# Kernel tuning notes

Measured on AMD Instinct MI355X. Metric: run time of the kernel, lower is better.

The kernel has to match this reference:

```python
import jax, jax.numpy as jnp
import numpy as np

B, N, D = 2, 4096, 1024
HID, OUT = 1024, 1
APPERTURE = 256
EPS = 1e-6
Q_SCALE = 0.06


def _ln(x, g, b):
    # torch.std defaults to unbiased (ddof=1); eps added to std, not var
    mean = x.mean(-1, keepdims=True)
    std = jnp.std(x, axis=-1, ddof=1, keepdims=True)
    return g * (x - mean) / (std + EPS) + b


def _self_attn(x, Wk, Wq, Wv, Wo):
    K = x @ Wk.T
    Q = (x @ Wq.T) * Q_SCALE
    V = x @ Wv.T
    logits = jnp.einsum('bnd,bmd->bnm', Q, K)  # [B,N,N]
    idx = jnp.arange(N)
    keep = jnp.abs(idx[:, None] - idx[None, :]) < APPERTURE  # band kept
    logits = jnp.where(keep[None], logits, -jnp.inf)
    w = jax.nn.softmax(logits, axis=-1)
    # torch: y = (V^T @ w)^T  == w^T applied column-wise -> einsum over first attn index
    y = jnp.einsum('bmn,bmd->bnd', w, V)
    return y @ Wo.T


def setup_inputs() -> dict:
    key = jax.random.key(0)
    ks = jax.random.split(key, 20)
    s = 0.02
    inp = {
        'x1': jax.random.normal(ks[0], (B, N, D), jnp.float32),
        'x2': jax.random.normal(ks[1], (B, N, D), jnp.float32),
        'x3': jax.random.normal(ks[2], (B, N, D), jnp.float32),
        'Wk': jax.random.normal(ks[3], (D, D), jnp.float32) * s,
        'Wq': jax.random.normal(ks[4], (D, D), jnp.float32) * s,
        'Wv': jax.random.normal(ks[5], (D, D), jnp.float32) * s,
        'Wo': jax.random.normal(ks[6], (D, D), jnp.float32) * s,
        'ka_w': jax.random.normal(ks[7], (HID, D), jnp.float32) * s,
        'ka_b': jnp.zeros((HID,), jnp.float32),
        'kb_w': jax.random.normal(ks[8], (HID, HID), jnp.float32) * s,
        'kb_b': jnp.zeros((HID,), jnp.float32),
        'kc_w': jax.random.normal(ks[9], (HID, HID), jnp.float32) * s,
        'kc_b': jnp.zeros((HID,), jnp.float32),
        'kd_w': jax.random.normal(ks[10], (OUT, HID), jnp.float32) * s,
        'kd_b': jnp.zeros((OUT,), jnp.float32),
        'g1': jnp.ones((D,), jnp.float32),
        'b1': jnp.zeros((D,), jnp.float32),
        'g2': jnp.ones((HID,), jnp.float32),
        'b2': jnp.zeros((HID,), jnp.float32),
    }
    return inp


def reference(x1, x2, x3, Wk, Wq, Wv, Wo, ka_w, ka_b, kb_w, kb_b,
              kc_w, kc_b, kd_w, kd_b, g1, b1, g2, b2):
    # dropout in eval mode -> identity
    y = jnp.zeros_like(x1)
    for x in (x1, x2, x3):
        a = _self_attn(x, Wk, Wq, Wv, Wo)
        y = y + _ln(a + x, g1, b1)
    y = y @ ka_w.T + ka_b
    y = y @ kb_w.T + kb_b
    y = y @ kc_w.T + kc_b
    y = jax.nn.relu(y)
    y = _ln(y, g2, b2)
    y = y @ kd_w.T + kd_b  # [B,N,1]
    return y.reshape(y.shape[0], -1)  # [B,N]
```

## Files before the change

### kernel.cpp

```cpp
#include <hip/hip_runtime.h>

#define NSEQ 4096
#define DDIM 1024
#define NROWS 8192
#define NROWS3 24576
#define BAND 512
#define BM 128
#define BN 128
#define BKT 64
#define PT_W 768
#define PT_CH 64

typedef __attribute__((ext_vector_type(8))) __bf16 bf16x8;
typedef __attribute__((ext_vector_type(4))) float f32x4;

__device__ __forceinline__ unsigned short f2b(float f) {
  unsigned int u = __float_as_uint(f);
  unsigned int r = (u + 0x7FFFu + ((u >> 16) & 1u)) >> 16;
  return (unsigned short)r;
}
__device__ __forceinline__ float b2f(unsigned short b) {
  return __uint_as_float(((unsigned int)b) << 16);
}

__device__ __forceinline__ void gload16(const unsigned short* g, unsigned short* l) {
  __builtin_amdgcn_global_load_lds(
      (const __attribute__((address_space(1))) void*)g,
      (__attribute__((address_space(3))) void*)l, 16, 0, 0);
}

__device__ __forceinline__ float blk_sum(float v) {
  __shared__ float red_s[4];
  #pragma unroll
  for (int o = 32; o; o >>= 1) v += __shfl_xor(v, o);
  __syncthreads();
  if ((threadIdx.x & 63) == 0) red_s[threadIdx.x >> 6] = v;
  __syncthreads();
  return red_s[0] + red_s[1] + red_s[2] + red_s[3];
}
__device__ __forceinline__ float blk_max(float v) {
  __shared__ float red_m[4];
  #pragma unroll
  for (int o = 32; o; o >>= 1) v = fmaxf(v, __shfl_xor(v, o));
  __syncthreads();
  if ((threadIdx.x & 63) == 0) red_m[threadIdx.x >> 6] = v;
  __syncthreads();
  return fmaxf(fmaxf(red_m[0], red_m[1]), fmaxf(red_m[2], red_m[3]));
}

__global__ __launch_bounds__(256) void k_cvt(const float* __restrict__ src,
                                             unsigned short* __restrict__ dst,
                                             int n4) {
  int i = blockIdx.x * 256 + threadIdx.x;
  if (i < n4) {
    float4 f = ((const float4*)src)[i];
    ushort4 o = make_ushort4(f2b(f.x), f2b(f.y), f2b(f.z), f2b(f.w));
    ((ushort4*)dst)[i] = o;
  }
}


__global__ __launch_bounds__(256) void k_gemm_qkv(
    const unsigned short* __restrict__ A,
    const unsigned short* __restrict__ W,
    unsigned short* __restrict__ Kout,
    unsigned short* __restrict__ Qout,
    unsigned short* __restrict__ Vtout)
{
  __shared__ unsigned short As[BM * BKT];
  __shared__ unsigned short Bs[BN * BKT];
  const int tid = threadIdx.x;
  const int lane = tid & 63, wave = tid >> 6;
  const int wm = wave >> 1, wn = wave & 1;
  const int lrow = lane & 15, kgrp = lane >> 4;
  const int srow = lane >> 3;
  const int sseg = (lane & 7) ^ srow;
  const size_t m0 = (size_t)blockIdx.x * BM;
  const size_t n0 = (size_t)blockIdx.y * BN;
  f32x4 acc[4][4] = {};

  for (int k0 = 0; k0 < DDIM; k0 += BKT) {
    #pragma unroll
    for (int i = 0; i < 4; ++i) {
      int chunk = wave * 4 + i;
      int row = chunk * 8 + srow;
      gload16(A + (m0 + row) * (size_t)DDIM + k0 + sseg * 8, As + chunk * 512);
      gload16(W + (n0 + row) * (size_t)DDIM + k0 + sseg * 8, Bs + chunk * 512);
    }
    __syncthreads();
    #pragma unroll
    for (int ks = 0; ks < 2; ++ks) {
      bf16x8 af[4], bfr[4];
      #pragma unroll
      for (int i = 0; i < 4; ++i)
        af[i] = *(const bf16x8*)&As[(wm * 64 + i * 16 + lrow) * BKT +
                                    (((ks * 4 + kgrp) ^ (lrow & 7)) << 3)];
      #pragma unroll
      for (int j = 0; j < 4; ++j)
        bfr[j] = *(const bf16x8*)&Bs[(wn * 64 + j * 16 + lrow) * BKT +
                                     (((ks * 4 + kgrp) ^ (lrow & 7)) << 3)];
      #pragma unroll
      for (int i = 0; i < 4; ++i)
        #pragma unroll
        for (int j = 0; j < 4; ++j)
          acc[i][j] = __builtin_amdgcn_mfma_f32_16x16x32_bf16(af[i], bfr[j], acc[i][j], 0, 0, 0);
    }
    __syncthreads();
  }

  const int seg = (int)(n0 >> 10);
  const float al = (seg == 1) ? 0.06f : 1.f;
  #pragma unroll
  for (int i = 0; i < 4; ++i) {
    int rbase = (int)m0 + wm * 64 + i * 16 + kgrp * 4;
    #pragma unroll
    for (int j = 0; j < 4; ++j) {
      int col = (int)n0 + wn * 64 + j * 16 + lrow;
      int d = col & 1023;
      if (seg == 2) {
        int z = rbase >> 12, nn = rbase & (NSEQ - 1);
        ushort4 o;
        o.x = f2b(acc[i][j][0]);
        o.y = f2b(acc[i][j][1]);
        o.z = f2b(acc[i][j][2]);
        o.w = f2b(acc[i][j][3]);
        *(ushort4*)&Vtout[((size_t)z * DDIM + d) * NSEQ + nn] = o;
      } else {
        unsigned short* dst = (seg == 1 ? Qout : Kout);
        #pragma unroll
        for (int r = 0; r < 4; ++r)
          dst[(size_t)(rbase + r) * DDIM + d] = f2b(acc[i][j][r] * al);
      }
    }
  }
}

__global__ __launch_bounds__(256) void k_gemm_bt(
    const unsigned short* __restrict__ A,
    const unsigned short* __restrict__ B,
    unsigned short* __restrict__ Cout,
    const float* __restrict__ bias, int relu)
{
  __shared__ unsigned short As[BM * BKT];
  __shared__ unsigned short Bs[BN * BKT];
  const int tid = threadIdx.x;
  const int lane = tid & 63, wave = tid >> 6;
  const int wm = wave >> 1, wn = wave & 1;
  const int lrow = lane & 15, kgrp = lane >> 4;
  const int srow = lane >> 3;
  const int sseg = (lane & 7) ^ srow;
  const size_t m0 = (size_t)blockIdx.x * BM;
  const size_t n0 = (size_t)blockIdx.y * BN;
  f32x4 acc[4][4] = {};

  for (int k0 = 0; k0 < DDIM; k0 += BKT) {
    #pragma unroll
    for (int i = 0; i < 4; ++i) {
      int chunk = wave * 4 + i;
      int row = chunk * 8 + srow;
      gload16(A + (m0 + row) * (size_t)DDIM + k0 + sseg * 8, As + chunk * 512);
      gload16(B + (n0 + row) * (size_t)DDIM + k0 + sseg * 8, Bs + chunk * 512);
    }
    __syncthreads();
    #pragma unroll
    for (int ks = 0; ks < 2; ++ks) {
      bf16x8 af[4], bfr[4];
      #pragma unroll
      for (int i = 0; i < 4; ++i)
        af[i] = *(const bf16x8*)&As[(wm * 64 + i * 16 + lrow) * BKT +
                                    (((ks * 4 + kgrp) ^ (lrow & 7)) << 3)];
      #pragma unroll
      for (int j = 0; j < 4; ++j)
        bfr[j] = *(const bf16x8*)&Bs[(wn * 64 + j * 16 + lrow) * BKT +
                                     (((ks * 4 + kgrp) ^ (lrow & 7)) << 3)];
      #pragma unroll
      for (int i = 0; i < 4; ++i)
        #pragma unroll
        for (int j = 0; j < 4; ++j)
          acc[i][j] = __builtin_amdgcn_mfma_f32_16x16x32_bf16(af[i], bfr[j], acc[i][j], 0, 0, 0);
    }
    __syncthreads();
  }

  #pragma unroll
  for (int i = 0; i < 4; ++i) {
    int rbase = (int)m0 + wm * 64 + i * 16 + kgrp * 4;
    #pragma unroll
    for (int j = 0; j < 4; ++j) {
      int col = (int)n0 + wn * 64 + j * 16 + lrow;
      float bv = bias ? bias[col] : 0.f;
      #pragma unroll
      for (int r = 0; r < 4; ++r) {
        float v = acc[i][j][r] + bv;
        if (relu) v = fmaxf(v, 0.f);
        Cout[(size_t)(rbase + r) * DDIM + col] = f2b(v);
      }
    }
  }
}

__global__ __launch_bounds__(256) void k_qk_banded(
    const unsigned short* __restrict__ Q,
    const unsigned short* __restrict__ Kmat,
    float* __restrict__ Sb)
{
  const int m0 = blockIdx.x * BM;
  const int n0 = m0 - 256 + blockIdx.y * BM;
  const int z = blockIdx.z;
  if (n0 + BM <= 0 || n0 >= NSEQ) return;
  const unsigned short* Ab = Q + (size_t)z * NSEQ * DDIM;
  const unsigned short* Bb = Kmat + (size_t)z * NSEQ * DDIM;
  __shared__ unsigned short As[BM * BKT];
  __shared__ unsigned short Bs[BN * BKT];
  const int tid = threadIdx.x;
  const int lane = tid & 63, wave = tid >> 6;
  const int wm = wave >> 1, wn = wave & 1;
  const int lrow = lane & 15, kgrp = lane >> 4;
  const int srow = lane >> 3;
  const int sseg = (lane & 7) ^ srow;
  f32x4 acc[4][4] = {};

  for (int k0 = 0; k0 < DDIM; k0 += BKT) {
    #pragma unroll
    for (int i = 0; i < 4; ++i) {
      int chunk = wave * 4 + i;
      int row = chunk * 8 + srow;
      gload16(Ab + (size_t)(m0 + row) * DDIM + k0 + sseg * 8, As + chunk * 512);
      int nr = n0 + row;
      nr = nr < 0 ? 0 : (nr >= NSEQ ? NSEQ - 1 : nr);
      gload16(Bb + (size_t)nr * DDIM + k0 + sseg * 8, Bs + chunk * 512);
    }
    __syncthreads();
    #pragma unroll
    for (int ks = 0; ks < 2; ++ks) {
      bf16x8 af[4], bfr[4];
      #pragma unroll
      for (int i = 0; i < 4; ++i)
        af[i] = *(const bf16x8*)&As[(wm * 64 + i * 16 + lrow) * BKT +
                                    (((ks * 4 + kgrp) ^ (lrow & 7)) << 3)];
      #pragma unroll
      for (int j = 0; j < 4; ++j)
        bfr[j] = *(const bf16x8*)&Bs[(wn * 64 + j * 16 + lrow) * BKT +
                                     (((ks * 4 + kgrp) ^ (lrow & 7)) << 3)];
      #pragma unroll
      for (int i = 0; i < 4; ++i)
        #pragma unroll
        for (int j = 0; j < 4; ++j)
          acc[i][j] = __builtin_amdgcn_mfma_f32_16x16x32_bf16(af[i], bfr[j], acc[i][j], 0, 0, 0);
    }
    __syncthreads();
  }

  float* Sz = Sb + (size_t)z * NSEQ * BAND;
  #pragma unroll
  for (int i = 0; i < 4; ++i) {
    #pragma unroll
    for (int j = 0; j < 4; ++j) {
      int n = n0 + wn * 64 + j * 16 + lrow;
      #pragma unroll
      for (int r = 0; r < 4; ++r) {
        int m = m0 + wm * 64 + i * 16 + kgrp * 4 + r;
        int dlt = n - m;
        if (n >= 0 && n < NSEQ && dlt >= -255 && dlt <= 255)
          Sz[(size_t)m * BAND + (dlt + 255)] = acc[i][j][r];
      }
    }
  }
}

__global__ __launch_bounds__(256) void k_softmax(
    const float* __restrict__ Sb, unsigned short* __restrict__ Pb)
{
  int row = blockIdx.x;
  int m = row & (NSEQ - 1);
  int tid = threadIdx.x;
  int jlo = max(0, 255 - m);
  int jhi = min(510, NSEQ - 1 - m + 255);
  const float* S = Sb + (size_t)row * BAND;
  int j0 = tid, j1 = tid + 256;
  bool ok0 = (j0 >= jlo) && (j0 <= jhi);
  bool ok1 = (j1 >= jlo) && (j1 <= jhi);
  float v0 = ok0 ? S[j0] : -1e30f;
  float v1 = ok1 ? S[j1] : -1e30f;
  float mx = blk_max(fmaxf(v0, v1));
  float e0 = ok0 ? __expf(v0 - mx) : 0.f;
  float e1 = ok1 ? __expf(v1 - mx) : 0.f;
  float sum = blk_sum(e0 + e1);
  float inv = 1.f / sum;
  unsigned short* P = Pb + (size_t)row * BAND;
  P[j0] = f2b(e0 * inv);
  P[j1] = f2b(e1 * inv);
}

__global__ __launch_bounds__(256) void k_transpose(
    const unsigned short* __restrict__ Pb, unsigned short* __restrict__ Pt)
{
  const int c = blockIdx.x;
  const int s = blockIdx.y;
  const int z = blockIdx.z;
  const unsigned short* Pbb = Pb + (size_t)z * NSEQ * BAND;
  unsigned short* Ptb = Pt + ((size_t)z * PT_CH + c) * PT_W * 64;
  __shared__ unsigned short Ts[64][130];
  const int t = threadIdx.x;
  const int half = t >> 7;
  const int jl = t & 127;
  #pragma unroll
  for (int e = 0; e < 32; ++e) {
    int mp = e * 2 + half;
    int j = s * 128 + jl - mp - 65;
    unsigned short v = 0;
    if (j >= 0 && j < BAND) v = Pbb[(size_t)(c * 64 + mp) * BAND + j];
    Ts[mp][jl] = v;
  }
  __syncthreads();
  const int nl = t >> 1;
  const int mg = t & 1;
  unsigned short* orow = Ptb + (size_t)(s * 128 + nl) * 64;
  #pragma unroll
  for (int v4 = 0; v4 < 4; ++v4) {
    int lc = mg * 4 + v4;
    int sc = lc ^ (nl & 7);
    __align__(16) unsigned short tmp[8];
    #pragma unroll
    for (int i = 0; i < 8; ++i) tmp[i] = Ts[lc * 8 + i][nl];
    *(uint4*)(orow + sc * 8) = *(const uint4*)tmp;
  }
}

__global__ __launch_bounds__(256) void k_pv(
    const unsigned short* __restrict__ Pt,
    const unsigned short* __restrict__ Vt,
    unsigned short* __restrict__ Y)
{
  const int n0 = blockIdx.x * BM;
  const int d0 = blockIdx.y * BN;
  const int z = blockIdx.z;
  const int tid = threadIdx.x;
  const int lane = tid & 63, wave = tid >> 6;
  const int wm = wave >> 1, wn = wave & 1;
  const int lrow = lane & 15, kgrp = lane >> 4;
  const int srow = lane >> 3;
  const int sseg = (lane & 7) ^ srow;
  __shared__ unsigned short As[BM * BKT];
  __shared__ unsigned short Bs[BN * BKT];
  f32x4 acc[4][4] = {};
  const unsigned short* Ptb = Pt + (size_t)z * PT_CH * PT_W * 64;
  const unsigned short* Vtb = Vt + (size_t)z * DDIM * NSEQ;

  for (int kk = 0; kk < 10; ++kk) {
    int mb = n0 - 256 + kk * 64;
    if (mb < 0 || mb >= NSEQ) continue;
    int c = mb >> 6;
    int np0 = 576 - kk * 64;
    const unsigned short* Abase = Ptb + ((size_t)c * PT_W + np0) * 64;
    #pragma unroll
    for (int i = 0; i < 4; ++i) {
      int chunk = wave * 4 + i;
      int row = chunk * 8 + srow;
      gload16(Abase + chunk * 512 + (size_t)lane * 8, As + chunk * 512);
      gload16(Vtb + (size_t)(d0 + row) * NSEQ + mb + sseg * 8, Bs + chunk * 512);
    }
    __syncthreads();
    #pragma unroll
    for (int ks = 0; ks < 2; ++ks) {
      bf16x8 af[4], bfr[4];
      #pragma unroll
      for (int i = 0; i < 4; ++i)
        af[i] = *(const bf16x8*)&As[(wm * 64 + i * 16 + lrow) * BKT +
                                    (((ks * 4 + kgrp) ^ (lrow & 7)) << 3)];
      #pragma unroll
      for (int j = 0; j < 4; ++j)
        bfr[j] = *(const bf16x8*)&Bs[(wn * 64 + j * 16 + lrow) * BKT +
                                     (((ks * 4 + kgrp) ^ (lrow & 7)) << 3)];
      #pragma unroll
      for (int i = 0; i < 4; ++i)
        #pragma unroll
        for (int j = 0; j < 4; ++j)
          acc[i][j] = __builtin_amdgcn_mfma_f32_16x16x32_bf16(af[i], bfr[j], acc[i][j], 0, 0, 0);
    }
    __syncthreads();
  }

  unsigned short* Yb = Y + (size_t)z * NSEQ * DDIM;
  #pragma unroll
  for (int i = 0; i < 4; ++i) {
    int nb = n0 + wm * 64 + i * 16 + kgrp * 4;
    #pragma unroll
    for (int j = 0; j < 4; ++j) {
      int d = d0 + wn * 64 + j * 16 + lrow;
      #pragma unroll
      for (int r = 0; r < 4; ++r)
        Yb[(size_t)(nb + r) * DDIM + d] = f2b(acc[i][j][r]);
    }
  }
}

__global__ __launch_bounds__(256) void k_ln3(
    const unsigned short* __restrict__ aB,
    const float* __restrict__ x1, const float* __restrict__ x2,
    const float* __restrict__ x3,
    const float* __restrict__ g, const float* __restrict__ bb,
    unsigned short* __restrict__ yB)
{
  int row = blockIdx.x;
  int tid = threadIdx.x;
  const float* xs[3] = {x1, x2, x3};
  float o[4] = {0.f, 0.f, 0.f, 0.f};
  float4 g4 = ((const float4*)g)[tid];
  float4 b4 = ((const float4*)bb)[tid];
  #pragma unroll
  for (int br = 0; br < 3; ++br) {
    const unsigned short* a = aB + (size_t)(br * NROWS + row) * DDIM;
    const float* x = xs[br] + (size_t)row * DDIM;
    ushort4 a4 = ((const ushort4*)a)[tid];
    float4 x4 = ((const float4*)x)[tid];
    float v[4];
    v[0] = b2f(a4.x) + x4.x;
    v[1] = b2f(a4.y) + x4.y;
    v[2] = b2f(a4.z) + x4.z;
    v[3] = b2f(a4.w) + x4.w;
    float mu = blk_sum(v[0] + v[1] + v[2] + v[3]) * (1.f / DDIM);
    float q = 0.f;
    #pragma unroll
    for (int i = 0; i < 4; ++i) { float d = v[i] - mu; q += d * d; }
    float var = blk_sum(q) * (1.f / (DDIM - 1));
    float inv = 1.f / (sqrtf(var) + 1e-6f);
    o[0] += g4.x * (v[0] - mu) * inv + b4.x;
    o[1] += g4.y * (v[1] - mu) * inv + b4.y;
    o[2] += g4.z * (v[2] - mu) * inv + b4.z;
    o[3] += g4.w * (v[3] - mu) * inv + b4.w;
  }
  ushort4 w = make_ushort4(f2b(o[0]), f2b(o[1]), f2b(o[2]), f2b(o[3]));
  ((ushort4*)(yB + (size_t)row * DDIM))[tid] = w;
}

__global__ __launch_bounds__(256) void k_ln_dot(
    const unsigned short* __restrict__ H,
    const float* __restrict__ g, const float* __restrict__ bb,
    const float* __restrict__ kw, const float* __restrict__ kb,
    float* __restrict__ out)
{
  int row = blockIdx.x;
  int tid = threadIdx.x;
  const unsigned short* h = H + (size_t)row * DDIM;
  ushort4 h4 = ((const ushort4*)h)[tid];
  float v[4] = {b2f(h4.x), b2f(h4.y), b2f(h4.z), b2f(h4.w)};
  float mu = blk_sum(v[0] + v[1] + v[2] + v[3]) * (1.f / DDIM);
  float q = 0.f;
  #pragma unroll
  for (int i = 0; i < 4; ++i) { float d = v[i] - mu; q += d * d; }
  float var = blk_sum(q) * (1.f / (DDIM - 1));
  float inv = 1.f / (sqrtf(var) + 1e-6f);
  float4 g4 = ((const float4*)g)[tid];
  float4 b4 = ((const float4*)bb)[tid];
  float4 k4 = ((const float4*)kw)[tid];
  float p = (g4.x * (v[0] - mu) * inv + b4.x) * k4.x
          + (g4.y * (v[1] - mu) * inv + b4.y) * k4.y
          + (g4.z * (v[2] - mu) * inv + b4.z) * k4.z
          + (g4.w * (v[3] - mu) * inv + b4.w) * k4.w;
  float tot = blk_sum(p);
  if (tid == 0) out[row] = tot + kb[0];
}

extern "C" void kernel_launch(void* const* d_in, const int* in_sizes, int n_in,
                              void* d_out, int out_size, void* d_ws, size_t ws_size,
                              hipStream_t stream)
{
  const float* x1 = (const float*)d_in[0];
  const float* x2 = (const float*)d_in[1];
  const float* x3 = (const float*)d_in[2];
  const float* Wk = (const float*)d_in[3];
  const float* Wq = (const float*)d_in[4];
  const float* Wv = (const float*)d_in[5];
  const float* Wo = (const float*)d_in[6];
  const float* ka_w = (const float*)d_in[7];
  const float* ka_b = (const float*)d_in[8];
  const float* kb_w = (const float*)d_in[9];
  const float* kb_b = (const float*)d_in[10];
  const float* kc_w = (const float*)d_in[11];
  const float* kc_b = (const float*)d_in[12];
  const float* kd_w = (const float*)d_in[13];
  const float* kd_b = (const float*)d_in[14];
  const float* g1 = (const float*)d_in[15];
  const float* b1 = (const float*)d_in[16];
  const float* g2 = (const float*)d_in[17];
  const float* b2 = (const float*)d_in[18];

  const size_t MB = 1024ull * 1024ull;
  char* base = (char*)d_ws;
  unsigned short* WkB = (unsigned short*)(base + 0 * MB);
  unsigned short* WoB = (unsigned short*)(base + 6 * MB);
  unsigned short* kaB = (unsigned short*)(base + 8 * MB);
  unsigned short* kbB = (unsigned short*)(base + 10 * MB);
  unsigned short* kcB = (unsigned short*)(base + 12 * MB);
  unsigned short* xB = (unsigned short*)(base + 14 * MB);
  float* Sb = (float*)(base + 14 * MB);
  unsigned short* aB = (unsigned short*)(base + 14 * MB);
  unsigned short* Kb = (unsigned short*)(base + 62 * MB);
  unsigned short* Pb = (unsigned short*)(base + 62 * MB);
  unsigned short* Ya = (unsigned short*)(base + 62 * MB);
  unsigned short* Qb = (unsigned short*)(base + 110 * MB);
  unsigned short* PtB = (unsigned short*)(base + 110 * MB);
  unsigned short* yB = (unsigned short*)(base + 110 * MB);
  unsigned short* h1 = (unsigned short*)(base + 126 * MB);
  unsigned short* h2 = (unsigned short*)(base + 142 * MB);
  unsigned short* VtB = (unsigned short*)(base + 158 * MB);
  unsigned short* h3 = (unsigned short*)(base + 158 * MB);
  (void)ws_size; (void)in_sizes; (void)n_in; (void)out_size;

  dim3 blk(256);
  const int W4 = (DDIM * DDIM) / 4;
  k_cvt<<<1024, blk, 0, stream>>>(Wk, WkB, W4);
  k_cvt<<<1024, blk, 0, stream>>>(Wq, WkB + 1024 * 1024, W4);
  k_cvt<<<1024, blk, 0, stream>>>(Wv, WkB + 2 * 1024 * 1024, W4);
  k_cvt<<<1024, blk, 0, stream>>>(Wo, WoB, W4);
  k_cvt<<<1024, blk, 0, stream>>>(ka_w, kaB, W4);
  k_cvt<<<1024, blk, 0, stream>>>(kb_w, kbB, W4);
  k_cvt<<<1024, blk, 0, stream>>>(kc_w, kcB, W4);

  const int X4 = (NROWS * DDIM) / 4;
  k_cvt<<<8192, blk, 0, stream>>>(x1, xB, X4);
  k_cvt<<<8192, blk, 0, stream>>>(x2, xB + (size_t)NROWS * DDIM, X4);
  k_cvt<<<8192, blk, 0, stream>>>(x3, xB + 2 * (size_t)NROWS * DDIM, X4);

  k_gemm_qkv<<<dim3(NROWS3 / BM, 3072 / BN), blk, 0, stream>>>(xB, WkB, Kb, Qb, VtB);
  k_qk_banded<<<dim3(NSEQ / BM, 5, 6), blk, 0, stream>>>(Qb, Kb, Sb);
  k_softmax<<<NROWS3, blk, 0, stream>>>(Sb, Pb);
  k_transpose<<<dim3(PT_CH, PT_W / 128, 6), blk, 0, stream>>>(Pb, PtB);
  k_pv<<<dim3(NSEQ / BM, DDIM / BN, 6), blk, 0, stream>>>(PtB, VtB, Ya);
  k_gemm_bt<<<dim3(NROWS3 / BM, DDIM / BN), blk, 0, stream>>>(Ya, WoB, aB, nullptr, 0);
  k_ln3<<<NROWS, blk, 0, stream>>>(aB, x1, x2, x3, g1, b1, yB);
  dim3 gm(NROWS / BM, DDIM / BN);
  k_gemm_bt<<<gm, blk, 0, stream>>>(yB, kaB, h1, ka_b, 0);
  k_gemm_bt<<<gm, blk, 0, stream>>>(h1, kbB, h2, kb_b, 0);
  k_gemm_bt<<<gm, blk, 0, stream>>>(h2, kcB, h3, kc_b, 1);
  k_ln_dot<<<NROWS, blk, 0, stream>>>(h3, g2, b2, kd_w, kd_b, (float*)d_out);
}
```

Measured before the change: 782.8 us.

## Replace dense GEMMs with 256x256 double-buffered tiled kernel and batch conversions

Measured after the change: 740.5 us. 5.4% less time.

```diff
diff --git a/kernel.cpp b/kernel.cpp
--- a/kernel.cpp
+++ b/kernel.cpp
@@ -48,152 +48,170 @@
   return fmaxf(fmaxf(red_m[0], red_m[1]), fmaxf(red_m[2], red_m[3]));
 }
 
-__global__ __launch_bounds__(256) void k_cvt(const float* __restrict__ src,
-                                             unsigned short* __restrict__ dst,
-                                             int n4) {
+__global__ __launch_bounds__(256) void k_cvt_w(
+    const float* __restrict__ w0, const float* __restrict__ w1,
+    const float* __restrict__ w2, const float* __restrict__ w3,
+    const float* __restrict__ w4, const float* __restrict__ w5,
+    const float* __restrict__ w6, unsigned short* __restrict__ dst)
+{
+  int y = blockIdx.y;
+  const float* src = (y == 0) ? w0 : (y == 1) ? w1 : (y == 2) ? w2 :
+                     (y == 3) ? w3 : (y == 4) ? w4 : (y == 5) ? w5 : w6;
   int i = blockIdx.x * 256 + threadIdx.x;
-  if (i < n4) {
-    float4 f = ((const float4*)src)[i];
-    ushort4 o = make_ushort4(f2b(f.x), f2b(f.y), f2b(f.z), f2b(f.w));
-    ((ushort4*)dst)[i] = o;
-  }
-}
-
-
-__global__ __launch_bounds__(256) void k_gemm_qkv(
+  float4 f = ((const float4*)src)[i];
+  ushort4 o = make_ushort4(f2b(f.x), f2b(f.y), f2b(f.z), f2b(f.w));
+  ((ushort4*)(dst + (size_t)y * DDIM * DDIM))[i] = o;
+}
+
+__global__ __launch_bounds__(256) void k_cvt3(
+    const float* __restrict__ x1, const float* __restrict__ x2,
+    const float* __restrict__ x3, unsigned short* __restrict__ dst)
+{
+  int y = blockIdx.y;
+  const float* src = (y == 0) ? x1 : (y == 1) ? x2 : x3;
+  int i = blockIdx.x * 256 + threadIdx.x;
+  float4 f = ((const float4*)src)[i];
+  ushort4 o = make_ushort4(f2b(f.x), f2b(f.y), f2b(f.z), f2b(f.w));
+  ((ushort4*)(dst + (size_t)y * NROWS * DDIM))[i] = o;
+}
+
+template<int OMODE>
+__global__ __launch_bounds__(512, 2) void k_gemm256(
     const unsigned short* __restrict__ A,
-    const unsigned short* __restrict__ W,
+    const unsigned short* __restrict__ B,
+    unsigned short* __restrict__ Cout,
+    const float* __restrict__ bias, int relu, int nby,
     unsigned short* __restrict__ Kout,
     unsigned short* __restrict__ Qout,
     unsigned short* __restrict__ Vtout)
 {
-  __shared__ unsigned short As[BM * BKT];
-  __shared__ unsigned short Bs[BN * BKT];
+  __shared__ unsigned short lds[65536];
   const int tid = threadIdx.x;
-  const int lane = tid & 63, wave = tid >> 6;
-  const int wm = wave >> 1, wn = wave & 1;
+  const int lane = tid & 63, wid = tid >> 6;
+  const int wm = wid >> 2, wn = wid & 3;
   const int lrow = lane & 15, kgrp = lane >> 4;
   const int srow = lane >> 3;
-  const int sseg = (lane & 7) ^ srow;
-  const size_t m0 = (size_t)blockIdx.x * BM;
-  const size_t n0 = (size_t)blockIdx.y * BN;
-  f32x4 acc[4][4] = {};
-
-  for (int k0 = 0; k0 < DDIM; k0 += BKT) {
-    #pragma unroll
-    for (int i = 0; i < 4; ++i) {
-      int chunk = wave * 4 + i;
-      int row = chunk * 8 + srow;
-      gload16(A + (m0 + row) * (size_t)DDIM + k0 + sseg * 8, As + chunk * 512);
-      gload16(W + (n0 + row) * (size_t)DDIM + k0 + sseg * 8, Bs + chunk * 512);
-    }
-    __syncthreads();
-    #pragma unroll
-    for (int ks = 0; ks < 2; ++ks) {
-      bf16x8 af[4], bfr[4];
-      #pragma unroll
-      for (int i = 0; i < 4; ++i)
-        af[i] = *(const bf16x8*)&As[(wm * 64 + i * 16 + lrow) * BKT +
-                                    (((ks * 4 + kgrp) ^ (lrow & 7)) << 3)];
-      #pragma unroll
-      for (int j = 0; j < 4; ++j)
-        bfr[j] = *(const bf16x8*)&Bs[(wn * 64 + j * 16 + lrow) * BKT +
-                                     (((ks * 4 + kgrp) ^ (lrow & 7)) << 3)];
-      #pragma unroll
-      for (int i = 0; i < 4; ++i)
+  const int schunk = (lane & 7) ^ srow;
+
+  const int nwg = gridDim.x;
+  const int q8 = nwg >> 3;
+  const int flat = blockIdx.x;
+  const int logical = (flat & 7) * q8 + (flat >> 3);
+  const size_t m0 = (size_t)(logical / nby) * 256;
+  const size_t n0 = (size_t)(logical % nby) * 256;
+
+  f32x4 acc[8][4] = {};
+
+  #define STAGE256(buf, k0)                                                   \
+    {                                                                         \
+      unsigned short* dA = lds + (buf) * 32768 + wid * 2048;                  \
+      unsigned short* dB = dA + 16384;                                        \
+      _Pragma("unroll")                                                       \
+      for (int l = 0; l < 4; ++l) {                                           \
+        int row = wid * 32 + l * 8 + srow;                                    \
+        gload16(A + (m0 + row) * 1024 + (k0) + schunk * 8, dA + l * 512);     \
+        gload16(B + (n0 + row) * 1024 + (k0) + schunk * 8, dB + l * 512);     \
+      }                                                                       \
+    }
+
+  STAGE256(0, 0)
+  STAGE256(1, 64)
+  asm volatile("s_waitcnt vmcnt(8)" ::: "memory");
+  __builtin_amdgcn_s_barrier();
+  __builtin_amdgcn_sched_barrier(0);
+
+  int cur = 0;
+  #pragma unroll 1
+  for (int t = 0; t < 16; ++t) {
+    const unsigned short* As = lds + cur * 32768;
+    const unsigned short* Bs = As + 16384;
+    #pragma unroll
+    for (int qn = 0; qn < 2; ++qn) {
+      bf16x8 bfr[2][2];
+      #pragma unroll
+      for (int j = 0; j < 2; ++j)
         #pragma unroll
-        for (int j = 0; j < 4; ++j)
-          acc[i][j] = __builtin_amdgcn_mfma_f32_16x16x32_bf16(af[i], bfr[j], acc[i][j], 0, 0, 0);
-    }
-    __syncthreads();
-  }
-
-  const int seg = (int)(n0 >> 10);
-  const float al = (seg == 1) ? 0.06f : 1.f;
-  #pragma unroll
-  for (int i = 0; i < 4; ++i) {
-    int rbase = (int)m0 + wm * 64 + i * 16 + kgrp * 4;
-    #pragma unroll
-    for (int j = 0; j < 4; ++j) {
-      int col = (int)n0 + wn * 64 + j * 16 + lrow;
-      int d = col & 1023;
-      if (seg == 2) {
-        int z = rbase >> 12, nn = rbase & (NSEQ - 1);
-        ushort4 o;
-        o.x = f2b(acc[i][j][0]);
-        o.y = f2b(acc[i][j][1]);
-        o.z = f2b(acc[i][j][2]);
-        o.w = f2b(acc[i][j][3]);
-        *(ushort4*)&Vtout[((size_t)z * DDIM + d) * NSEQ + nn] = o;
-      } else {
-        unsigned short* dst = (seg == 1 ? Qout : Kout);
+        for (int ks = 0; ks < 2; ++ks) {
+          int rb = wn * 64 + qn * 32 + j * 16 + lrow;
+          bfr[j][ks] = *(const bf16x8*)&Bs[rb * 64 + (((ks * 4 + kgrp) ^ (rb & 7)) << 3)];
+        }
+      #pragma unroll
+      for (int qm = 0; qm < 2; ++qm) {
+        bf16x8 af[4][2];
         #pragma unroll
-        for (int r = 0; r < 4; ++r)
-          dst[(size_t)(rbase + r) * DDIM + d] = f2b(acc[i][j][r] * al);
+        for (int i = 0; i < 4; ++i)
+          #pragma unroll
+          for (int ks = 0; ks < 2; ++ks) {
+            int ra = wm * 128 + qm * 64 + i * 16 + lrow;
+            af[i][ks] = *(const bf16x8*)&As[ra * 64 + (((ks * 4 + kgrp) ^ (ra & 7)) << 3)];
+          }
+        __builtin_amdgcn_s_setprio(1);
+        #pragma unroll
+        for (int i = 0; i < 4; ++i)
+          #pragma unroll
+          for (int j = 0; j < 2; ++j)
+            #pragma unroll
+            for (int ks = 0; ks < 2; ++ks)
+              acc[qm * 4 + i][qn * 2 + j] = __builtin_amdgcn_mfma_f32_16x16x32_bf16(
+                  af[i][ks], bfr[j][ks], acc[qm * 4 + i][qn * 2 + j], 0, 0, 0);
+        __builtin_amdgcn_s_setprio(0);
       }
     }
-  }
-}
-
-__global__ __launch_bounds__(256) void k_gemm_bt(
-    const unsigned short* __restrict__ A,
-    const unsigned short* __restrict__ B,
-    unsigned short* __restrict__ Cout,
-    const float* __restrict__ bias, int relu)
-{
-  __shared__ unsigned short As[BM * BKT];
-  __shared__ unsigned short Bs[BN * BKT];
-  const int tid = threadIdx.x;
-  const int lane = tid & 63, wave = tid >> 6;
-  const int wm = wave >> 1, wn = wave & 1;
-  const int lrow = lane & 15, kgrp = lane >> 4;
-  const int srow = lane >> 3;
-  const int sseg = (lane & 7) ^ srow;
-  const size_t m0 = (size_t)blockIdx.x * BM;
-  const size_t n0 = (size_t)blockIdx.y * BN;
-  f32x4 acc[4][4] = {};
-
-  for (int k0 = 0; k0 < DDIM; k0 += BKT) {
-    #pragma unroll
-    for (int i = 0; i < 4; ++i) {
-      int chunk = wave * 4 + i;
-      int row = chunk * 8 + srow;
-      gload16(A + (m0 + row) * (size_t)DDIM + k0 + sseg * 8, As + chunk * 512);
-      gload16(B + (n0 + row) * (size_t)DDIM + k0 + sseg * 8, Bs + chunk * 512);
-    }
-    __syncthreads();
-    #pragma unroll
-    for (int ks = 0; ks < 2; ++ks) {
-      bf16x8 af[4], bfr[4];
-      #pragma unroll
-      for (int i = 0; i < 4; ++i)
-        af[i] = *(const bf16x8*)&As[(wm * 64 + i * 16 + lrow) * BKT +
-                                    (((ks * 4 + kgrp) ^ (lrow & 7)) << 3)];
-      #pragma unroll
-      for (int j = 0; j < 4; ++j)
-        bfr[j] = *(const bf16x8*)&Bs[(wn * 64 + j * 16 + lrow) * BKT +
-                                     (((ks * 4 + kgrp) ^ (lrow & 7)) << 3)];
-      #pragma unroll
-      for (int i = 0; i < 4; ++i)
+    if (t == 15) break;
+    __builtin_amdgcn_s_barrier();
+    __builtin_amdgcn_sched_barrier(0);
+    if (t < 14) {
+      STAGE256(cur, (t + 2) * 64)
+      asm volatile("s_waitcnt vmcnt(8)" ::: "memory");
+    } else {
+      asm volatile("s_waitcnt vmcnt(0)" ::: "memory");
+    }
+    __builtin_amdgcn_s_barrier();
+    __builtin_amdgcn_sched_barrier(0);
+    cur ^= 1;
+  }
+  #undef STAGE256
+
+  if (OMODE == 1) {
+    const int seg = (int)(n0 >> 10);
+    const float al = (seg == 1) ? 0.06f : 1.f;
+    #pragma unroll
+    for (int ai = 0; ai < 8; ++ai) {
+      int rbase = (int)m0 + wm * 128 + (ai >> 2) * 64 + (ai & 3) * 16 + kgrp * 4;
+      #pragma unroll
+      for (int bj = 0; bj < 4; ++bj) {
+        int col = (int)n0 + wn * 64 + (bj >> 1) * 32 + (bj & 1) * 16 + lrow;
+        int d = col & 1023;
+        if (seg == 2) {
+          int z = rbase >> 12, nn = rbase & (NSEQ - 1);
+          ushort4 o;
+          o.x = f2b(acc[ai][bj][0]);
+          o.y = f2b(acc[ai][bj][1]);
+          o.z = f2b(acc[ai][bj][2]);
+          o.w = f2b(acc[ai][bj][3]);
+          *(ushort4*)&Vtout[((size_t)z * DDIM + d) * NSEQ + nn] = o;
+        } else {
+          unsigned short* dst = (seg == 1 ? Qout : Kout);
+          #pragma unroll
+          for (int r = 0; r < 4; ++r)
+            dst[(size_t)(rbase + r) * DDIM + d] = f2b(acc[ai][bj][r] * al);
+        }
+      }
+    }
+  } else {
+    #pragma unroll
+    for (int ai = 0; ai < 8; ++ai) {
+      int rbase = (int)m0 + wm * 128 + (ai >> 2) * 64 + (ai & 3) * 16 + kgrp * 4;
+      #pragma unroll
+      for (int bj = 0; bj < 4; ++bj) {
+        int col = (int)n0 + wn * 64 + (bj >> 1) * 32 + (bj & 1) * 16 + lrow;
+        float bv = bias ? bias[col] : 0.f;
         #pragma unroll
-        for (int j = 0; j < 4; ++j)
-          acc[i][j] = __builtin_amdgcn_mfma_f32_16x16x32_bf16(af[i], bfr[j], acc[i][j], 0, 0, 0);
-    }
-    __syncthreads();
-  }
-
-  #pragma unroll
-  for (int i = 0; i < 4; ++i) {
-    int rbase = (int)m0 + wm * 64 + i * 16 + kgrp * 4;
-    #pragma unroll
-    for (int j = 0; j < 4; ++j) {
-      int col = (int)n0 + wn * 64 + j * 16 + lrow;
-      float bv = bias ? bias[col] : 0.f;
-      #pragma unroll
-      for (int r = 0; r < 4; ++r) {
-        float v = acc[i][j][r] + bv;
-        if (relu) v = fmaxf(v, 0.f);
-        Cout[(size_t)(rbase + r) * DDIM + col] = f2b(v);
+        for (int r = 0; r < 4; ++r) {
+          float v = acc[ai][bj][r] + bv;
+          if (relu) v = fmaxf(v, 0.f);
+          Cout[(size_t)(rbase + r) * 1024 + col] = f2b(v);
+        }
       }
     }
   }
@@ -420,10 +438,10 @@
     v[2] = b2f(a4.z) + x4.z;
     v[3] = b2f(a4.w) + x4.w;
     float mu = blk_sum(v[0] + v[1] + v[2] + v[3]) * (1.f / DDIM);
-    float q = 0.f;
-    #pragma unroll
-    for (int i = 0; i < 4; ++i) { float d = v[i] - mu; q += d * d; }
-    float var = blk_sum(q) * (1.f / (DDIM - 1));
+    float qq = 0.f;
+    #pragma unroll
+    for (int i = 0; i < 4; ++i) { float d = v[i] - mu; qq += d * d; }
+    float var = blk_sum(qq) * (1.f / (DDIM - 1));
     float inv = 1.f / (sqrtf(var) + 1e-6f);
     o[0] += g4.x * (v[0] - mu) * inv + b4.x;
     o[1] += g4.y * (v[1] - mu) * inv + b4.y;
@@ -446,10 +464,10 @@
   ushort4 h4 = ((const ushort4*)h)[tid];
   float v[4] = {b2f(h4.x), b2f(h4.y), b2f(h4.z), b2f(h4.w)};
   float mu = blk_sum(v[0] + v[1] + v[2] + v[3]) * (1.f / DDIM);
-  float q = 0.f;
-  #pragma unroll
-  for (int i = 0; i < 4; ++i) { float d = v[i] - mu; q += d * d; }
-  float var = blk_sum(q) * (1.f / (DDIM - 1));
+  float qq = 0.f;
+  #pragma unroll
+  for (int i = 0; i < 4; ++i) { float d = v[i] - mu; qq += d * d; }
+  float var = blk_sum(qq) * (1.f / (DDIM - 1));
   float inv = 1.f / (sqrtf(var) + 1e-6f);
   float4 g4 = ((const float4*)g)[tid];
   float4 b4 = ((const float4*)bb)[tid];
@@ -508,31 +526,24 @@
   unsigned short* h3 = (unsigned short*)(base + 158 * MB);
   (void)ws_size; (void)in_sizes; (void)n_in; (void)out_size;
 
-  dim3 blk(256);
-  const int W4 = (DDIM * DDIM) / 4;
-  k_cvt<<<1024, blk, 0, stream>>>(Wk, WkB, W4);
-  k_cvt<<<1024, blk, 0, stream>>>(Wq, WkB + 1024 * 1024, W4);
-  k_cvt<<<1024, blk, 0, stream>>>(Wv, WkB + 2 * 1024 * 1024, W4);
-  k_cvt<<<1024, blk, 0, stream>>>(Wo, WoB, W4);
-  k_cvt<<<1024, blk, 0, stream>>>(ka_w, kaB, W4);
-  k_cvt<<<1024, blk, 0, stream>>>(kb_w, kbB, W4);
-  k_cvt<<<1024, blk, 0, stream>>>(kc_w, kcB, W4);
-
-  const int X4 = (NROWS * DDIM) / 4;
-  k_cvt<<<8192, blk, 0, stream>>>(x1, xB, X4);
-  k_cvt<<<8192, blk, 0, stream>>>(x2, xB + (size_t)NROWS * DDIM, X4);
-  k_cvt<<<8192, blk, 0, stream>>>(x3, xB + 2 * (size_t)NROWS * DDIM, X4);
-
-  k_gemm_qkv<<<dim3(NROWS3 / BM, 3072 / BN), blk, 0, stream>>>(xB, WkB, Kb, Qb, VtB);
+  dim3 blk(256), blk5(512);
+  k_cvt_w<<<dim3(1024, 7), blk, 0, stream>>>(Wk, Wq, Wv, Wo, ka_w, kb_w, kc_w, WkB);
+  k_cvt3<<<dim3(8192, 3), blk, 0, stream>>>(x1, x2, x3, xB);
+
+  k_gemm256<1><<<dim3(96 * 12), blk5, 0, stream>>>(xB, WkB, nullptr, nullptr, 0, 12,
+                                                   Kb, Qb, VtB);
   k_qk_banded<<<dim3(NSEQ / BM, 5, 6), blk, 0, stream>>>(Qb, Kb, Sb);
   k_softmax<<<NROWS3, blk, 0, stream>>>(Sb, Pb);
   k_transpose<<<dim3(PT_CH, PT_W / 128, 6), blk, 0, stream>>>(Pb, PtB);
   k_pv<<<dim3(NSEQ / BM, DDIM / BN, 6), blk, 0, stream>>>(PtB, VtB, Ya);
-  k_gemm_bt<<<dim3(NROWS3 / BM, DDIM / BN), blk, 0, stream>>>(Ya, WoB, aB, nullptr, 0);
+  k_gemm256<0><<<dim3(96 * 4), blk5, 0, stream>>>(Ya, WoB, aB, nullptr, 0, 4,
+                                                  nullptr, nullptr, nullptr);
   k_ln3<<<NROWS, blk, 0, stream>>>(aB, x1, x2, x3, g1, b1, yB);
-  dim3 gm(NROWS / BM, DDIM / BN);
-  k_gemm_bt<<<gm, blk, 0, stream>>>(yB, kaB, h1, ka_b, 0);
-  k_gemm_bt<<<gm, blk, 0, stream>>>(h1, kbB, h2, kb_b, 0);
-  k_gemm_bt<<<gm, blk, 0, stream>>>(h2, kcB, h3, kc_b, 1);
+  k_gemm256<0><<<dim3(32 * 4), blk5, 0, stream>>>(yB, kaB, h1, ka_b, 0, 4,
+                                                  nullptr, nullptr, nullptr);
+  k_gemm256<0><<<dim3(32 * 4), blk5, 0, stream>>>(h1, kbB, h2, kb_b, 0, 4,
+                                                  nullptr, nullptr, nullptr);
+  k_gemm256<0><<<dim3(32 * 4), blk5, 0, stream>>>(h2, kcB, h3, kc_b, 1, 4,
+                                                  nullptr, nullptr, nullptr);
   k_ln_dot<<<NROWS, blk, 0, stream>>>(h3, g2, b2, kd_w, kd_b, (float*)d_out);
 }
```
